# Kernel tuning notes

Hardware: AMD Instinct MI355X
Metric: run time of the kernel (lower is better)

## Reference

```python
import jax, jax.numpy as jnp
import numpy as np

B, L, D = 2, 4096, 1024
H, DK, DV = 4, 256, 256
CONV_K, FIR_S, FIR_L = 4, 3, 31
CHUNK = 32
EPS = 1e-5


def l2norm(x):
    return x * jax.lax.rsqrt(jnp.sum(x * x, -1, keepdims=True) + 1e-6)


def causal_dwconv(x, w):
    # x: [B, L, C], w: [C, K] depthwise causal FIR conv (left pad K-1)
    C, K = w.shape
    y = jax.lax.conv_general_dilated(
        jnp.swapaxes(x, 1, 2), w[:, None, :], (1,), [(K - 1, 0)],
        feature_group_count=C, dimension_numbers=('NCH', 'OIH', 'NCH'))
    return jnp.swapaxes(y, 1, 2)


def delta_rule_chunkwise(q, k, v, beta, chunk=CHUNK):
    # q,k: [b,h,L,dk], v: [b,h,L,dv], beta: [b,h,L]
    b, h, Lx, dk = q.shape
    dv = v.shape[-1]
    pad = (-Lx) % chunk
    if pad:
        q, k, v = (jnp.pad(t, ((0, 0), (0, 0), (0, pad), (0, 0))) for t in (q, k, v))
        beta = jnp.pad(beta, ((0, 0), (0, 0), (0, pad)))
    Lp = Lx + pad
    n = Lp // chunk
    q = l2norm(q)
    k = l2norm(k)
    v = v * beta[..., None]
    k_beta = k * beta[..., None]
    ch = lambda t: t.reshape(b, h, n, chunk, -1)
    qc, kc, vc, kbc = map(ch, (q, k, v, k_beta))
    # UT transform: T = (I + strictly_lower(k_beta @ k^T))^{-1}
    A = jnp.einsum('bhncd,bhned->bhnce', kbc, kc)
    eye = jnp.eye(chunk, dtype=q.dtype)
    T = jnp.linalg.inv(eye + jnp.tril(A, -1))  # same math as the sequential forward-substitution loop
    u = T @ vc      # [b,h,n,c,dv]
    w = T @ kbc     # [b,h,n,c,dk]
    tri = jnp.tril(jnp.ones((chunk, chunk), bool))  # causal incl. diagonal

    def body(S, inp):
        q_i, k_i, u_i, w_i = inp
        attn = jnp.where(tri, jnp.einsum('bhcd,bhed->bhce', q_i, k_i), 0.)
        u_i = u_i - w_i @ S
        o_i = q_i @ S + attn @ u_i
        S = S + jnp.einsum('bhcd,bhce->bhde', k_i, u_i)
        return S, o_i

    mv = lambda t: jnp.moveaxis(t, 2, 0)
    S0 = jnp.zeros((b, h, dk, dv), q.dtype)
    S, o = jax.lax.scan(body, S0, (mv(qc), mv(kc), mv(u), mv(w)))
    o = jnp.moveaxis(o, 0, 2).reshape(b, h, Lp, dv)[:, :, :Lx]
    return o, S


def setup_inputs() -> dict:
    key = jax.random.key(0)
    ks = jax.random.split(key, 16)
    s = 0.02
    fir_short = jnp.zeros((H, DV, FIR_S)).at[..., -1].set(1.0) + 1e-3 * jax.random.normal(ks[8], (H, DV, FIR_S))
    fir_long = jnp.zeros((H, DV, FIR_L)).at[..., -1].set(1.0) + 1e-3 * jax.random.normal(ks[9], (H, DV, FIR_L))
    bl = jnp.zeros((H, 3)).at[:, 0].set(2.0).reshape(-1)  # value_path_bias
    return dict(
        hidden_states=jax.random.normal(ks[0], (B, L, D), jnp.float32),
        Wq=s * jax.random.normal(ks[1], (D, H * DK)),
        Wk=s * jax.random.normal(ks[2], (D, H * DK)),
        Wv=s * jax.random.normal(ks[3], (D, H * DV)),
        conv_q=0.3 * jax.random.normal(ks[4], (H * DK, CONV_K)),
        conv_k=0.3 * jax.random.normal(ks[5], (H * DK, CONV_K)),
        conv_v=0.3 * jax.random.normal(ks[6], (H * DV, CONV_K)),
        Wb=s * jax.random.normal(ks[7], (D, H)),
        fir_short=fir_short,
        fir_long=fir_long,
        Wg=s * jax.random.normal(ks[10], (D, H)),
        bg=0.5 * jnp.ones((H,)),  # global_gate_bias
        Wl=s * jax.random.normal(ks[11], (D, H * 3)),
        bl=bl,
        log_temp=jnp.ones((H,)),  # log(e * temp_init) with temp_init=1
        rms_w=jnp.ones((DV,)),
        Wo=s * jax.random.normal(ks[12], (H * DV, D)),
    )


def reference(hidden_states, Wq, Wk, Wv, conv_q, conv_k, conv_v, Wb,
              fir_short, fir_long, Wg, bg, Wl, bl, log_temp, rms_w, Wo):
    x = hidden_states
    Bx, Lx, _ = x.shape
    # q/k/v projections + causal short conv + SiLU (qk_activation='silu')
    q = jax.nn.silu(causal_dwconv(x @ Wq, conv_q)).reshape(Bx, Lx, H, DK)
    k = jax.nn.silu(causal_dwconv(x @ Wk, conv_k)).reshape(Bx, Lx, H, DK)
    v = jax.nn.silu(causal_dwconv(x @ Wv, conv_v)).reshape(Bx, Lx, H, DV)
    beta = jax.nn.sigmoid(x @ Wb)  # [B,L,H]
    o_d, S = delta_rule_chunkwise(
        q.transpose(0, 2, 1, 3), k.transpose(0, 2, 1, 3),
        v.transpose(0, 2, 1, 3), beta.transpose(0, 2, 1))
    delta_out = o_d.transpose(0, 2, 1, 3)  # [B,L,H,DV]
    # local FIR paths on v (per-head depthwise causal FIR)
    vf = v.reshape(Bx, Lx, H * DV)
    local_short = causal_dwconv(vf, fir_short.reshape(H * DV, FIR_S)).reshape(Bx, Lx, H, DV)
    local_long = causal_dwconv(vf, fir_long.reshape(H * DV, FIR_L)).reshape(Bx, Lx, H, DV)
    # hierarchical two-stage gating with learnable per-head temperature
    w_global = jax.nn.sigmoid(x @ Wg + bg)  # [B,L,H]
    temp = jnp.exp(log_temp)                # [H]
    logits = (x @ Wl + bl).reshape(Bx, Lx, H, 3) / temp[:, None]
    p = jax.nn.softmax(logits, axis=-1)
    local_mix = p[..., 0:1] * v + p[..., 1:2] * local_short + p[..., 2:3] * local_long
    o = w_global[..., None] * delta_out + (1.0 - w_global)[..., None] * local_mix
    # per-head RMSNorm then output projection
    o = o * jax.lax.rsqrt(jnp.mean(o * o, -1, keepdims=True) + EPS) * rms_w
    return o.reshape(Bx, Lx, H * DV) @ Wo
```

## Files before the change

### kernel.cpp

```cpp
#include <hip/hip_runtime.h>
#include <hip/hip_bf16.h>
#include <math.h>

#define Bn 2
#define Ln 4096
#define Dn 1024
#define Hn 4
#define DKn 256
#define DVn 256
#define NCHn 128

typedef __attribute__((ext_vector_type(8))) short short8;
typedef __attribute__((ext_vector_type(4))) float f32x4;

__device__ __forceinline__ float sigmoidf_(float x) { return 1.f / (1.f + __expf(-x)); }

__device__ __forceinline__ unsigned short f2bf(float f) {
  union { float f; unsigned u; } v; v.f = f;
  unsigned r = v.u + 0x7FFFu + ((v.u >> 16) & 1u);
  return (unsigned short)(r >> 16);
}

__device__ __forceinline__ unsigned cvt_pk_bf16(float a, float b) {
  unsigned r;
  asm volatile("v_cvt_pk_bf16_f32 %0, %1, %2" : "=v"(r) : "v"(a), "v"(b));
  return r;
}

__device__ __forceinline__ short8 pack_i4(int4 o) {
  short8 r;
  __builtin_memcpy(&r, &o, 16);
  return r;
}

__device__ __forceinline__ void gl2lds16(const void* g, void* l) {
  __builtin_amdgcn_global_load_lds((const __attribute__((address_space(1))) unsigned int*)g,
                                   (__attribute__((address_space(3))) unsigned int*)l, 16, 0, 0);
}

__global__ __launch_bounds__(256) void wt_kernel(const float* __restrict__ W,
                                                 unsigned short* __restrict__ Wt,
                                                 int K, int N) {
  __shared__ float tile[32][33];
  const int bx = blockIdx.x * 32;
  const int by = blockIdx.y * 32;
  const int tx = threadIdx.x & 31, ty4 = (threadIdx.x >> 5) * 4;
#pragma unroll
  for (int r = 0; r < 4; ++r)
    tile[ty4 + r][tx] = W[(size_t)(by + ty4 + r) * N + bx + tx];
  __syncthreads();
#pragma unroll
  for (int r = 0; r < 4; ++r)
    Wt[(size_t)(bx + ty4 + r) * K + by + tx] = f2bf(tile[tx][ty4 + r]);
}

__global__ __launch_bounds__(256) void f2bf_kernel(const float* __restrict__ in,
                                                   unsigned short* __restrict__ out,
                                                   int n) {
  const int i4 = (blockIdx.x * 256 + threadIdx.x) * 4;
  if (i4 >= n) return;
  const float4 v = *(const float4*)&in[i4];
  ushort4 o;
  o.x = f2bf(v.x); o.y = f2bf(v.y); o.z = f2bf(v.z); o.w = f2bf(v.w);
  *(ushort4*)&out[i4] = o;
}

__global__ __launch_bounds__(256, 2) void gemm_bf16(const unsigned short* __restrict__ A,
                                                    const unsigned short* __restrict__ Bt,
                                                    float* __restrict__ C,
                                                    int M, int N, int K) {
  __shared__ __align__(16) unsigned short As[128 * 32];
  __shared__ __align__(16) unsigned short Bs[128 * 32];
  const int tid = threadIdx.x;
  const int wid = tid >> 6, lane = tid & 63;
  const int row0 = blockIdx.y * 128, col0 = blockIdx.x * 128;
  const int wr64 = (wid >> 1) * 64, wc64 = (wid & 1) * 64;
  const int fr = lane & 15, fg = lane >> 4;
  f32x4 acc[4][4];
#pragma unroll
  for (int i = 0; i < 4; ++i)
#pragma unroll
    for (int j = 0; j < 4; ++j) acc[i][j] = (f32x4){0.f, 0.f, 0.f, 0.f};
  for (int k0 = 0; k0 < K; k0 += 32) {
#pragma unroll
    for (int i = 0; i < 2; ++i) {
      const int off = wid * 2048 + i * 1024 + (lane << 4);
      const int r = off >> 6;
      const int kb = off & 63;
      gl2lds16((const char*)A + ((size_t)(row0 + r) * K + k0) * 2 + kb, (char*)As + off);
      gl2lds16((const char*)Bt + ((size_t)(col0 + r) * K + k0) * 2 + kb, (char*)Bs + off);
    }
    __syncthreads();
    short8 a[4], b[4];
#pragma unroll
    for (int mi = 0; mi < 4; ++mi)
      a[mi] = *(const short8*)&As[(wr64 + mi * 16 + fr) * 32 + fg * 8];
#pragma unroll
    for (int ni = 0; ni < 4; ++ni)
      b[ni] = *(const short8*)&Bs[(wc64 + ni * 16 + fr) * 32 + fg * 8];
#pragma unroll
    for (int mi = 0; mi < 4; ++mi)
#pragma unroll
      for (int ni = 0; ni < 4; ++ni)
        acc[mi][ni] = __builtin_amdgcn_mfma_f32_16x16x32_bf16(a[mi], b[ni], acc[mi][ni], 0, 0, 0);
    __syncthreads();
  }
#pragma unroll
  for (int mi = 0; mi < 4; ++mi) {
    const int orow = row0 + wr64 + mi * 16 + fg * 4;
#pragma unroll
    for (int ni = 0; ni < 4; ++ni) {
      const int ocol = col0 + wc64 + ni * 16 + fr;
#pragma unroll
      for (int r = 0; r < 4; ++r)
        C[(size_t)(orow + r) * N + ocol] = acc[mi][ni][r];
    }
  }
}

__global__ __launch_bounds__(256) void gates_kernel(
    const float* __restrict__ x, const float* __restrict__ Wb,
    const float* __restrict__ Wg, const float* __restrict__ bg,
    const float* __restrict__ Wl, const float* __restrict__ bl,
    const float* __restrict__ log_temp, float* __restrict__ beta,
    float* __restrict__ wgl, float* __restrict__ pmix) {
  const int wave = threadIdx.x >> 6, lane = threadIdx.x & 63;
  const int row = (blockIdx.x << 2) + wave;
  if (row >= Bn * Ln) return;
  const float* xr = x + (size_t)row * Dn;
  float acc[20];
#pragma unroll
  for (int c = 0; c < 20; ++c) acc[c] = 0.f;
#pragma unroll
  for (int i = 0; i < 4; ++i) {
    const float4 xv = *(const float4*)&xr[(lane << 2) + (i << 8)];
    const float xa[4] = {xv.x, xv.y, xv.z, xv.w};
#pragma unroll
    for (int j = 0; j < 4; ++j) {
      const int kk = (i << 8) + (lane << 2) + j;
      const float xx = xa[j];
#pragma unroll
      for (int h = 0; h < 4; ++h) acc[h] = fmaf(xx, Wb[kk * 4 + h], acc[h]);
#pragma unroll
      for (int h = 0; h < 4; ++h) acc[4 + h] = fmaf(xx, Wg[kk * 4 + h], acc[4 + h]);
#pragma unroll
      for (int c = 0; c < 12; ++c) acc[8 + c] = fmaf(xx, Wl[kk * 12 + c], acc[8 + c]);
    }
  }
#pragma unroll
  for (int c = 0; c < 20; ++c)
    for (int off = 32; off; off >>= 1) acc[c] += __shfl_down(acc[c], off);
  if (lane == 0) {
    const int b = row >> 12, l = row & (Ln - 1);
#pragma unroll
    for (int h = 0; h < 4; ++h)
      beta[((size_t)(b * Hn + h) << 12) + l] = sigmoidf_(acc[h]);
#pragma unroll
    for (int h = 0; h < 4; ++h) wgl[row * 4 + h] = sigmoidf_(acc[4 + h] + bg[h]);
#pragma unroll
    for (int h = 0; h < 4; ++h) {
      const float it = 1.f / __expf(log_temp[h]);
      const float l0 = (acc[8 + h * 3 + 0] + bl[h * 3 + 0]) * it;
      const float l1 = (acc[8 + h * 3 + 1] + bl[h * 3 + 1]) * it;
      const float l2 = (acc[8 + h * 3 + 2] + bl[h * 3 + 2]) * it;
      const float mx = fmaxf(l0, fmaxf(l1, l2));
      const float e0 = __expf(l0 - mx), e1 = __expf(l1 - mx), e2 = __expf(l2 - mx);
      const float is = 1.f / (e0 + e1 + e2);
      pmix[row * 12 + h * 3 + 0] = e0 * is;
      pmix[row * 12 + h * 3 + 1] = e1 * is;
      pmix[row * 12 + h * 3 + 2] = e2 * is;
    }
  }
}

template <int DO_L2>
__global__ __launch_bounds__(256) void conv_act_kernel(
    const float* __restrict__ raw, const float* __restrict__ cw,
    float* __restrict__ out, int coloff) {
  const int blk = blockIdx.x;
  const int b = blk >> 12, l = blk & (Ln - 1);
  const int t = threadIdx.x;
  float vals[4];
#pragma unroll
  for (int g = 0; g < 4; ++g) {
    const int c = (g << 8) + t;
    float a = 0.f;
#pragma unroll
    for (int j = 0; j < 4; ++j) {
      const int ls = l - 3 + j;
      if (ls >= 0)
        a = fmaf(cw[c * 4 + j], raw[(((size_t)b << 12) + ls) * 3072 + coloff + c], a);
    }
    vals[g] = a * sigmoidf_(a);
  }
  if (DO_L2) {
    __shared__ float red[4][4];
    float ss[4];
#pragma unroll
    for (int g = 0; g < 4; ++g) ss[g] = vals[g] * vals[g];
#pragma unroll
    for (int g = 0; g < 4; ++g)
      for (int off = 32; off; off >>= 1) ss[g] += __shfl_down(ss[g], off);
    const int wave = t >> 6, lane = t & 63;
    if (lane == 0) {
#pragma unroll
      for (int g = 0; g < 4; ++g) red[wave][g] = ss[g];
    }
    __syncthreads();
#pragma unroll
    for (int g = 0; g < 4; ++g) {
      const float s = red[0][g] + red[1][g] + red[2][g] + red[3][g];
      vals[g] *= rsqrtf(s + 1e-6f);
    }
  }
#pragma unroll
  for (int g = 0; g < 4; ++g)
    out[((((size_t)(b * Hn + g)) << 12) + l) * 256 + t] = vals[g];
}

__global__ __launch_bounds__(256, 2) void precomp_kernel(
    const float* __restrict__ q, const float* __restrict__ k,
    const float* __restrict__ v, const float* __restrict__ beta,
    unsigned short* __restrict__ wfrag, unsigned short* __restrict__ qfrag,
    unsigned short* __restrict__ ktfrag, unsigned short* __restrict__ afrag,
    float* __restrict__ u0frag) {
  const int blk = blockIdx.x;
  const int n = blk & 127, bh = blk >> 7;
  const size_t base = (((size_t)bh << 12) + (n << 5)) * 256;
  const size_t cid = (size_t)(bh * NCHn + n);
  __shared__ __align__(16) unsigned short ksb[32][264];
  __shared__ __align__(16) unsigned short qsb[32][264];
  __shared__ __align__(16) unsigned short vbb[32][264];
  __shared__ float Tm[32][33], Am[32][33], bet[32];
  __shared__ __align__(16) float attn_l[32][36];
  const int t = threadIdx.x;
  const int wid = t >> 6, lane = t & 63;
  const int fr = lane & 15, fg = lane >> 4;
  if (t < 32) bet[t] = beta[((size_t)bh << 12) + (n << 5) + t];
#pragma unroll
  for (int it = 0; it < 4; ++it) {
    const int idx = t + it * 256;
    const int r = idx >> 5, c8 = (idx & 31) << 3;
    const float bv = beta[((size_t)bh << 12) + (n << 5) + r];
    const float4 q0 = *(const float4*)&q[base + r * 256 + c8];
    const float4 q1 = *(const float4*)&q[base + r * 256 + c8 + 4];
    const float4 k0 = *(const float4*)&k[base + r * 256 + c8];
    const float4 k1 = *(const float4*)&k[base + r * 256 + c8 + 4];
    const float4 v0 = *(const float4*)&v[base + r * 256 + c8];
    const float4 v1 = *(const float4*)&v[base + r * 256 + c8 + 4];
    int4 oq, ok, ov;
    oq.x = cvt_pk_bf16(q0.x, q0.y); oq.y = cvt_pk_bf16(q0.z, q0.w);
    oq.z = cvt_pk_bf16(q1.x, q1.y); oq.w = cvt_pk_bf16(q1.z, q1.w);
    ok.x = cvt_pk_bf16(k0.x, k0.y); ok.y = cvt_pk_bf16(k0.z, k0.w);
    ok.z = cvt_pk_bf16(k1.x, k1.y); ok.w = cvt_pk_bf16(k1.z, k1.w);
    ov.x = cvt_pk_bf16(v0.x * bv, v0.y * bv); ov.y = cvt_pk_bf16(v0.z * bv, v0.w * bv);
    ov.z = cvt_pk_bf16(v1.x * bv, v1.y * bv); ov.w = cvt_pk_bf16(v1.z * bv, v1.w * bv);
    *(int4*)&qsb[r][c8] = oq;
    *(int4*)&ksb[r][c8] = ok;
    *(int4*)&vbb[r][c8] = ov;
  }
  __syncthreads();
  {
    const int ti = wid >> 1, tj = wid & 1;
    f32x4 G = (f32x4){0.f, 0.f, 0.f, 0.f};
    f32x4 At = (f32x4){0.f, 0.f, 0.f, 0.f};
#pragma unroll
    for (int kw = 0; kw < 8; ++kw) {
      const short8 krow = *(const short8*)&ksb[ti * 16 + fr][kw * 32 + fg * 8];
      const short8 kcol = *(const short8*)&ksb[tj * 16 + fr][kw * 32 + fg * 8];
      const short8 qrow = *(const short8*)&qsb[ti * 16 + fr][kw * 32 + fg * 8];
      G = __builtin_amdgcn_mfma_f32_16x16x32_bf16(krow, kcol, G, 0, 0, 0);
      At = __builtin_amdgcn_mfma_f32_16x16x32_bf16(qrow, kcol, At, 0, 0, 0);
    }
#pragma unroll
    for (int r_ = 0; r_ < 4; ++r_) {
      const int i = ti * 16 + fg * 4 + r_;
      const int j = tj * 16 + fr;
      Am[i][j] = bet[i] * G[r_];
      attn_l[i][j] = (j <= i) ? At[r_] : 0.f;
    }
  }
#pragma unroll
  for (int it = 0; it < 4; ++it) {
    const int u = it * 4 + wid;
    const int mi = u >> 3, kw = u & 7;
    *(int4*)&qfrag[cid * 8192 + u * 512 + lane * 8] =
        *(const int4*)&qsb[mi * 16 + fr][kw * 32 + fg * 8];
  }
#pragma unroll
  for (int it = 0; it < 4; ++it) {
    const int mi = it * 4 + wid;
    const int dk = mi * 16 + fr;
    unsigned short e[8];
#pragma unroll
    for (int j = 0; j < 8; ++j) e[j] = ksb[fg * 8 + j][dk];
    int4 o;
    o.x = e[0] | ((unsigned)e[1] << 16);
    o.y = e[2] | ((unsigned)e[3] << 16);
    o.z = e[4] | ((unsigned)e[5] << 16);
    o.w = e[6] | ((unsigned)e[7] << 16);
    *(int4*)&ktfrag[cid * 8192 + mi * 512 + lane * 8] = o;
  }
  __syncthreads();
  if (t >= 128) {
    const int mi = (t >> 6) - 2;
    const int c = mi * 16 + fr;
    const float4 a = *(const float4*)&attn_l[c][fg * 8];
    const float4 b2 = *(const float4*)&attn_l[c][fg * 8 + 4];
    int4 o;
    o.x = f2bf(a.x) | ((unsigned)f2bf(a.y) << 16);
    o.y = f2bf(a.z) | ((unsigned)f2bf(a.w) << 16);
    o.z = f2bf(b2.x) | ((unsigned)f2bf(b2.y) << 16);
    o.w = f2bf(b2.z) | ((unsigned)f2bf(b2.w) << 16);
    *(int4*)&afrag[cid * 1024 + mi * 512 + lane * 8] = o;
  }
  if (t < 32) {
    float Tcol[32];
    Tcol[0] = (t == 0) ? 1.f : 0.f;
#pragma unroll
    for (int i = 1; i < 32; ++i) {
      float s0 = 0.f, s1 = 0.f;
      int m = 0;
#pragma unroll
      for (; m + 2 <= i; m += 2) {
        s0 = fmaf(Am[i][m], Tcol[m], s0);
        s1 = fmaf(Am[i][m + 1], Tcol[m + 1], s1);
      }
      if (m < i) s0 = fmaf(Am[i][m], Tcol[m], s0);
      Tcol[i] = ((i == t) ? 1.f : 0.f) - s0 - s1;
    }
#pragma unroll
    for (int i = 0; i < 32; ++i) Tm[i][t] = Tcol[i];
  }
  __syncthreads();
  {
    float betr[8];
#pragma unroll
    for (int j = 0; j < 8; ++j) betr[j] = bet[fg * 8 + j];
    short8 Tf[2], Tbf[2];
#pragma unroll
    for (int mi = 0; mi < 2; ++mi) {
      float tv[8];
#pragma unroll
      for (int j = 0; j < 8; ++j) tv[j] = Tm[mi * 16 + fr][fg * 8 + j];
      int4 p, pb;
      p.x = cvt_pk_bf16(tv[0], tv[1]); p.y = cvt_pk_bf16(tv[2], tv[3]);
      p.z = cvt_pk_bf16(tv[4], tv[5]); p.w = cvt_pk_bf16(tv[6], tv[7]);
      pb.x = cvt_pk_bf16(tv[0] * betr[0], tv[1] * betr[1]);
      pb.y = cvt_pk_bf16(tv[2] * betr[2], tv[3] * betr[3]);
      pb.z = cvt_pk_bf16(tv[4] * betr[4], tv[5] * betr[5]);
      pb.w = cvt_pk_bf16(tv[6] * betr[6], tv[7] * betr[7]);
      Tf[mi] = pack_i4(p);
      Tbf[mi] = pack_i4(pb);
    }
    const f32x4 zero = (f32x4){0.f, 0.f, 0.f, 0.f};
#pragma unroll
    for (int tt = 0; tt < 4; ++tt) {
      const int tjc = wid * 4 + tt;
      unsigned short ev[8], ek[8];
#pragma unroll
      for (int j = 0; j < 8; ++j) {
        ev[j] = vbb[fg * 8 + j][tjc * 16 + fr];
        ek[j] = ksb[fg * 8 + j][tjc * 16 + fr];
      }
      int4 pv, pk;
      pv.x = ev[0] | ((unsigned)ev[1] << 16); pv.y = ev[2] | ((unsigned)ev[3] << 16);
      pv.z = ev[4] | ((unsigned)ev[5] << 16); pv.w = ev[6] | ((unsigned)ev[7] << 16);
      pk.x = ek[0] | ((unsigned)ek[1] << 16); pk.y = ek[2] | ((unsigned)ek[3] << 16);
      pk.z = ek[4] | ((unsigned)ek[5] << 16); pk.w = ek[6] | ((unsigned)ek[7] << 16);
      const short8 vbf = pack_i4(pv);
      const short8 kbf = pack_i4(pk);
#pragma unroll
      for (int mi = 0; mi < 2; ++mi) {
        const f32x4 U = __builtin_amdgcn_mfma_f32_16x16x32_bf16(Tf[mi], vbf, zero, 0, 0, 0);
        *(f32x4*)&u0frag[cid * 8192 + (tjc * 2 + mi) * 256 + lane * 4] = U;
        const f32x4 W = __builtin_amdgcn_mfma_f32_16x16x32_bf16(Tbf[mi], kbf, zero, 0, 0, 0);
#pragma unroll
        for (int r_ = 0; r_ < 4; ++r_)
          qsb[mi * 16 + fg * 4 + r_][tjc * 16 + fr] = f2bf(W[r_]);
      }
    }
  }
  __syncthreads();
#pragma unroll
  for (int it = 0; it < 4; ++it) {
    const int u = it * 4 + wid;
    const int mi = u >> 3, kw = u & 7;
    *(int4*)&wfrag[cid * 8192 + u * 512 + lane * 8] =
        *(const int4*)&qsb[mi * 16 + fr][kw * 32 + fg * 8];
  }
}

__global__ __launch_bounds__(128, 1) void scan_mfma(
    const unsigned short* __restrict__ wfrag, const unsigned short* __restrict__ qfrag,
    const unsigned short* __restrict__ ktfrag, const unsigned short* __restrict__ afrag,
    const float* __restrict__ u0frag, float* __restrict__ dout) {
  const int bh = blockIdx.x & 7;
  const int dvs = blockIdx.x >> 3;
  const int tid = threadIdx.x;
  const int w = tid >> 6;
  const int lane = tid & 63;
  const int fr = lane & 15, fg = lane >> 4;
  const int swz = (fr & 7) << 4;
  __shared__ __align__(16) unsigned short St[2][2048];
  __shared__ __align__(16) unsigned short ut2[2][512];
  __shared__ __align__(16) float pux[2][2][2][256];
  __shared__ __align__(16) float pox[2][2][2][256];
  f32x4 S[8];
#pragma unroll
  for (int i = 0; i < 8; ++i) S[i] = (f32x4){0.f, 0.f, 0.f, 0.f};

  const unsigned short* wbase = wfrag + (size_t)(bh * NCHn) * 8192;
  const unsigned short* qbase = qfrag + (size_t)(bh * NCHn) * 8192;
  const unsigned short* kbase = ktfrag + (size_t)(bh * NCHn) * 8192;
  const unsigned short* abase = afrag + (size_t)(bh * NCHn) * 1024;
  const float* ubase = u0frag + (size_t)(bh * NCHn) * 8192 + dvs * 512;

  short8 wr[8], qr[8], ktr[8];
  short8 ar[2] = {};
  f32x4 u0r[2];
#pragma unroll
  for (int u8 = 0; u8 < 8; ++u8) {
    const int mi = u8 >> 2, kwp = u8 & 3;
    const int u = mi * 8 + 4 * w + kwp;
    wr[u8] = *(const short8*)&wbase[u * 512 + lane * 8];
    qr[u8] = *(const short8*)&qbase[u * 512 + lane * 8];
    ktr[u8] = *(const short8*)&kbase[(8 * w + u8) * 512 + lane * 8];
  }
#pragma unroll
  for (int u = 0; u < 2; ++u) u0r[u] = *(const f32x4*)&ubase[u * 256 + lane * 4];
  if (w == 0) {
#pragma unroll
    for (int u = 0; u < 2; ++u) ar[u] = *(const short8*)&abase[u * 512 + lane * 8];
  }

  for (int n = 0; n < NCHn; ++n) {
    const int np = (n + 1 < NCHn) ? (n + 1) : n;
    const int buf = n & 1;
#pragma unroll
    for (int mi = 0; mi < 8; ++mi) {
      const unsigned w0 = cvt_pk_bf16(S[mi][0], S[mi][1]);
      const unsigned w1 = cvt_pk_bf16(S[mi][2], S[mi][3]);
      const int a = (fr * 256 + mi * 32 + fg * 8) ^ swz;
      *(uint2*)((char*)&St[w][0] + a) = make_uint2(w0, w1);
    }
    short8 sb[4];
#pragma unroll
    for (int kwp = 0; kwp < 4; ++kwp) {
      const int a = (fr * 256 + kwp * 64 + fg * 16) ^ swz;
      sb[kwp] = *(const short8*)((const char*)&St[w][0] + a);
    }
    f32x4 up[2], oq[2];
    up[0] = up[1] = (f32x4){0.f, 0.f, 0.f, 0.f};
    oq[0] = oq[1] = (f32x4){0.f, 0.f, 0.f, 0.f};
#pragma unroll
    for (int kwp = 0; kwp < 4; ++kwp) {
#pragma unroll
      for (int mi = 0; mi < 2; ++mi) {
        up[mi] = __builtin_amdgcn_mfma_f32_16x16x32_bf16(wr[mi * 4 + kwp], sb[kwp], up[mi], 0, 0, 0);
        oq[mi] = __builtin_amdgcn_mfma_f32_16x16x32_bf16(qr[mi * 4 + kwp], sb[kwp], oq[mi], 0, 0, 0);
      }
    }
    {
      const unsigned short* wp = wbase + (size_t)np * 8192;
      const unsigned short* qp = qbase + (size_t)np * 8192;
#pragma unroll
      for (int u8 = 0; u8 < 8; ++u8) {
        const int mi = u8 >> 2, kwp = u8 & 3;
        const int u = mi * 8 + 4 * w + kwp;
        wr[u8] = *(const short8*)&wp[u * 512 + lane * 8];
        qr[u8] = *(const short8*)&qp[u * 512 + lane * 8];
      }
    }
#pragma unroll
    for (int mi = 0; mi < 2; ++mi) {
      *(f32x4*)&pux[w][buf][mi][lane * 4] = up[mi];
      *(f32x4*)&pox[w][buf][mi][lane * 4] = oq[mi];
    }
    asm volatile("s_waitcnt lgkmcnt(0)" ::: "memory");
    __builtin_amdgcn_s_barrier();
    __builtin_amdgcn_sched_barrier(0);
    f32x4 o_f[2];
#pragma unroll
    for (int mi = 0; mi < 2; ++mi) {
      const f32x4 puo = *(const f32x4*)&pux[w ^ 1][buf][mi][lane * 4];
      const f32x4 uu = u0r[mi] - up[mi] - puo;
      const unsigned a0 = cvt_pk_bf16(uu[0], uu[1]);
      const unsigned a1 = cvt_pk_bf16(uu[2], uu[3]);
      const int ad = (fr * 64 + mi * 32 + fg * 8) ^ swz;
      *(uint2*)((char*)&ut2[w][0] + ad) = make_uint2(a0, a1);
      o_f[mi] = oq[mi] + *(const f32x4*)&pox[w ^ 1][buf][mi][lane * 4];
    }
    asm volatile("s_waitcnt lgkmcnt(0)" ::: "memory");
    __builtin_amdgcn_sched_barrier(0);
    const short8 ub = *(const short8*)((const char*)&ut2[w][0] + ((fr * 64 + fg * 16) ^ swz));
    if (w == 0) {
#pragma unroll
      for (int mi = 0; mi < 2; ++mi)
        o_f[mi] = __builtin_amdgcn_mfma_f32_16x16x32_bf16(ar[mi], ub, o_f[mi], 0, 0, 0);
      const unsigned short* ap = abase + (size_t)np * 1024;
#pragma unroll
      for (int u = 0; u < 2; ++u) ar[u] = *(const short8*)&ap[u * 512 + lane * 8];
      const size_t cb = ((size_t)((bh << 12) + (n << 5))) * 256;
#pragma unroll
      for (int mi = 0; mi < 2; ++mi)
#pragma unroll
        for (int r = 0; r < 4; ++r)
          dout[cb + (size_t)(mi * 16 + fg * 4 + r) * 256 + dvs * 16 + fr] = o_f[mi][r];
    }
    {
      const float* up_ = ubase + (size_t)np * 8192;
#pragma unroll
      for (int u = 0; u < 2; ++u) u0r[u] = *(const f32x4*)&up_[u * 256 + lane * 4];
    }
#pragma unroll
    for (int mi = 0; mi < 8; ++mi)
      S[mi] = __builtin_amdgcn_mfma_f32_16x16x32_bf16(ktr[mi], ub, S[mi], 0, 0, 0);
    {
      const unsigned short* kp = kbase + (size_t)np * 8192;
#pragma unroll
      for (int u8 = 0; u8 < 8; ++u8)
        ktr[u8] = *(const short8*)&kp[(8 * w + u8) * 512 + lane * 8];
    }
  }
}

#define MIX_LT 16
__global__ __launch_bounds__(256) void mix_kernel(
    const float* __restrict__ v, const float* __restrict__ delta,
    const float* __restrict__ wgl, const float* __restrict__ pmix,
    const float* __restrict__ firs, const float* __restrict__ firl,
    const float* __restrict__ rms_w, unsigned short* __restrict__ out) {
  const int wgid = ((int)blockIdx.x & 7) * 256 + ((int)blockIdx.x >> 3);
  const int b = wgid >> 10;
  const int h = (wgid >> 8) & 3;
  const int lt = wgid & 255;
  const int l0 = lt * MIX_LT;
  const int t = threadIdx.x;
  const int wv = t >> 6, lane = t & 63;
  const float* vcol = v + ((((size_t)(b * Hn + h)) << 12)) * 256 + t;
  const float* dcol = delta + ((((size_t)(b * Hn + h)) << 12)) * 256 + t;
  float fw[31], fs3[3];
#pragma unroll
  for (int j = 0; j < 31; ++j) fw[j] = firl[((h << 8) + t) * 31 + j];
#pragma unroll
  for (int j = 0; j < 3; ++j) fs3[j] = firs[((h << 8) + t) * 3 + j];
  const float rw = rms_w[t];
  float vbuf[46];
#pragma unroll
  for (int j = 0; j < 30; ++j) {
    const int ls = l0 - 30 + j;
    vbuf[j] = (ls >= 0) ? vcol[(size_t)ls * 256] : 0.f;
  }
#pragma unroll
  for (int i = 0; i < MIX_LT; ++i) vbuf[30 + i] = vcol[(size_t)(l0 + i) * 256];
  __shared__ float wred[MIX_LT * 4];
  float o[MIX_LT];
#pragma unroll
  for (int i = 0; i < MIX_LT; ++i) {
    const int l = l0 + i;
    const float vnew = vbuf[30 + i];
    float lo = fw[30] * vnew;
#pragma unroll
    for (int j = 0; j < 30; ++j) lo = fmaf(fw[j], vbuf[i + j], lo);
    float sh = fs3[2] * vnew;
    sh = fmaf(fs3[1], vbuf[i + 29], sh);
    sh = fmaf(fs3[0], vbuf[i + 28], sh);
    const int row = (b << 12) + l;
    const float p0 = pmix[row * 12 + h * 3 + 0];
    const float p1 = pmix[row * 12 + h * 3 + 1];
    const float p2 = pmix[row * 12 + h * 3 + 2];
    const float wg = wgl[row * 4 + h];
    const float mixv = p0 * vnew + p1 * sh + p2 * lo;
    const float oo = wg * dcol[(size_t)l * 256] + (1.f - wg) * mixv;
    o[i] = oo;
    float ss = oo * oo;
#pragma unroll
    for (int m = 1; m < 64; m <<= 1) ss += __shfl_xor(ss, m);
    if (lane == 0) wred[i * 4 + wv] = ss;
  }
  __syncthreads();
#pragma unroll
  for (int i = 0; i < MIX_LT; ++i) {
    const float sum = wred[i * 4] + wred[i * 4 + 1] + wred[i * 4 + 2] + wred[i * 4 + 3];
    const float sc = rsqrtf(sum * (1.f / 256.f) + 1e-5f);
    const int l = l0 + i;
    out[(size_t)((b << 12) + l) * 1024 + (h << 8) + t] = f2bf(o[i] * sc * rw);
  }
}

extern "C" void kernel_launch(void* const* d_in, const int* in_sizes, int n_in,
                              void* d_out, int out_size, void* d_ws, size_t ws_size,
                              hipStream_t stream) {
  const float* x = (const float*)d_in[0];
  const float* Wq = (const float*)d_in[1];
  const float* Wk = (const float*)d_in[2];
  const float* Wv = (const float*)d_in[3];
  const float* cq = (const float*)d_in[4];
  const float* ck = (const float*)d_in[5];
  const float* cv = (const float*)d_in[6];
  const float* Wb = (const float*)d_in[7];
  const float* firs = (const float*)d_in[8];
  const float* firl = (const float*)d_in[9];
  const float* Wg = (const float*)d_in[10];
  const float* bg = (const float*)d_in[11];
  const float* Wl = (const float*)d_in[12];
  const float* bl = (const float*)d_in[13];
  const float* ltemp = (const float*)d_in[14];
  const float* rmsw = (const float*)d_in[15];
  const float* Wo = (const float*)d_in[16];

  float* ws = (float*)d_ws;
  const size_t NE = (size_t)Bn * Ln * 1024;
  float* qkvraw = ws;
  float* kraw = ws + NE;
  float* vraw = ws + 2 * NE;
  float* qn = ws + 3 * NE;
  float* kn = ws + 4 * NE;
  float* vn = ws + 5 * NE;
  float* beta = ws + 6 * NE;
  float* wgl = beta + (size_t)Bn * Hn * Ln;
  float* pmix = wgl + (size_t)Bn * Ln * Hn;
  float* attn_unused = pmix + (size_t)Bn * Ln * Hn * 3;
  unsigned short* Wot = (unsigned short*)(attn_unused + (size_t)Bn * Hn * NCHn * 1024);
  unsigned short* xb = (unsigned short*)qn;
  unsigned short* Wqt = (unsigned short*)(qn + 4194304);
  unsigned short* Wkt = Wqt + 1048576;
  unsigned short* Wvt = Wkt + 1048576;
  unsigned short* normed_bf = (unsigned short*)kn;
  unsigned short* wfrag = (unsigned short*)qkvraw;
  unsigned short* qfrag = wfrag + 8388608;
  unsigned short* ktfrag = (unsigned short*)kraw;
  unsigned short* afrag = ktfrag + 8388608;
  float* u0frag = qn;
  float* dbuf = vraw;

  const dim3 wtg(32, 32);
  wt_kernel<<<wtg, 256, 0, stream>>>(Wq, Wqt, 1024, 1024);
  wt_kernel<<<wtg, 256, 0, stream>>>(Wk, Wkt, 1024, 1024);
  wt_kernel<<<wtg, 256, 0, stream>>>(Wv, Wvt, 1024, 1024);
  wt_kernel<<<wtg, 256, 0, stream>>>(Wo, Wot, 1024, 1024);
  f2bf_kernel<<<(int)(NE / 1024), 256, 0, stream>>>(x, xb, (int)NE);

  gemm_bf16<<<dim3(24, 64), 256, 0, stream>>>(xb, Wqt, qkvraw, Bn * Ln, 3072, 1024);
  gates_kernel<<<Bn * Ln / 4, 256, 0, stream>>>(x, Wb, Wg, bg, Wl, bl, ltemp,
                                                beta, wgl, pmix);
  conv_act_kernel<1><<<Bn * Ln, 256, 0, stream>>>(qkvraw, cq, qn, 0);
  conv_act_kernel<1><<<Bn * Ln, 256, 0, stream>>>(qkvraw, ck, kn, 1024);
  conv_act_kernel<0><<<Bn * Ln, 256, 0, stream>>>(qkvraw, cv, vn, 2048);
  precomp_kernel<<<Bn * Hn * NCHn, 256, 0, stream>>>(qn, kn, vn, beta, wfrag,
                                                     qfrag, ktfrag, afrag, u0frag);
  scan_mfma<<<128, 128, 0, stream>>>(wfrag, qfrag, ktfrag, afrag, u0frag, dbuf);
  mix_kernel<<<Bn * Hn * (Ln / MIX_LT), 256, 0, stream>>>(
      vn, dbuf, wgl, pmix, firs, firl, rmsw, normed_bf);
  gemm_bf16<<<dim3(8, 64), 256, 0, stream>>>(normed_bf, Wot, (float*)d_out,
                                             Bn * Ln, 1024, 1024);
}
```

Before: 458.4 us.

## Store intermediates in bf16 and fuse weight transposes and x conversion

Stores the QKV projection output, the conv-activated q/k/v, and the delta-rule output as bf16 instead of fp32, roughly halving intermediate memory traffic across the conv, precompute, scan and mix kernels. The four weight-transpose launches are merged into one 3D-grid kernel, and the x-to-bf16 conversion is folded into the gates kernel, removing a standalone pass. The workspace layout is reorganised to match. This adds bf16 rounding before the conv/SiLU/L2 norm and before the mix, which could reduce accuracy.

Result: faster. 444.6 us (-3.0%).

```diff
diff --git a/kernel.cpp b/kernel.cpp
--- a/kernel.cpp
+++ b/kernel.cpp
@@ -21,6 +21,11 @@
   return (unsigned short)(r >> 16);
 }
 
+__device__ __forceinline__ float bf2f(unsigned short u) {
+  union { unsigned u; float f; } v; v.u = ((unsigned)u) << 16;
+  return v.f;
+}
+
 __device__ __forceinline__ unsigned cvt_pk_bf16(float a, float b) {
   unsigned r;
   asm volatile("v_cvt_pk_bf16_f32 %0, %1, %2" : "=v"(r) : "v"(a), "v"(b));
@@ -38,36 +43,32 @@
                                    (__attribute__((address_space(3))) unsigned int*)l, 16, 0, 0);
 }
 
-__global__ __launch_bounds__(256) void wt_kernel(const float* __restrict__ W,
-                                                 unsigned short* __restrict__ Wt,
-                                                 int K, int N) {
+__global__ __launch_bounds__(256) void wt_all_kernel(
+    const float* __restrict__ W0, const float* __restrict__ W1,
+    const float* __restrict__ W2, const float* __restrict__ W3,
+    unsigned short* __restrict__ T0, unsigned short* __restrict__ T1,
+    unsigned short* __restrict__ T2, unsigned short* __restrict__ T3) {
+  const float* W = (blockIdx.z == 0) ? W0 : (blockIdx.z == 1) ? W1
+                   : (blockIdx.z == 2) ? W2 : W3;
+  unsigned short* Wt = (blockIdx.z == 0) ? T0 : (blockIdx.z == 1) ? T1
+                       : (blockIdx.z == 2) ? T2 : T3;
   __shared__ float tile[32][33];
   const int bx = blockIdx.x * 32;
   const int by = blockIdx.y * 32;
   const int tx = threadIdx.x & 31, ty4 = (threadIdx.x >> 5) * 4;
 #pragma unroll
   for (int r = 0; r < 4; ++r)
-    tile[ty4 + r][tx] = W[(size_t)(by + ty4 + r) * N + bx + tx];
+    tile[ty4 + r][tx] = W[(size_t)(by + ty4 + r) * 1024 + bx + tx];
   __syncthreads();
 #pragma unroll
   for (int r = 0; r < 4; ++r)
-    Wt[(size_t)(bx + ty4 + r) * K + by + tx] = f2bf(tile[tx][ty4 + r]);
-}
-
-__global__ __launch_bounds__(256) void f2bf_kernel(const float* __restrict__ in,
-                                                   unsigned short* __restrict__ out,
-                                                   int n) {
-  const int i4 = (blockIdx.x * 256 + threadIdx.x) * 4;
-  if (i4 >= n) return;
-  const float4 v = *(const float4*)&in[i4];
-  ushort4 o;
-  o.x = f2bf(v.x); o.y = f2bf(v.y); o.z = f2bf(v.z); o.w = f2bf(v.w);
-  *(ushort4*)&out[i4] = o;
-}
-
+    Wt[(size_t)(bx + ty4 + r) * 1024 + by + tx] = f2bf(tile[tx][ty4 + r]);
+}
+
+template <int OBF>
 __global__ __launch_bounds__(256, 2) void gemm_bf16(const unsigned short* __restrict__ A,
                                                     const unsigned short* __restrict__ Bt,
-                                                    float* __restrict__ C,
+                                                    void* __restrict__ Cv,
                                                     int M, int N, int K) {
   __shared__ __align__(16) unsigned short As[128 * 32];
   __shared__ __align__(16) unsigned short Bs[128 * 32];
@@ -111,9 +112,17 @@
 #pragma unroll
     for (int ni = 0; ni < 4; ++ni) {
       const int ocol = col0 + wc64 + ni * 16 + fr;
-#pragma unroll
-      for (int r = 0; r < 4; ++r)
-        C[(size_t)(orow + r) * N + ocol] = acc[mi][ni][r];
+      if (OBF) {
+        unsigned short* C = (unsigned short*)Cv;
+#pragma unroll
+        for (int r = 0; r < 4; ++r)
+          C[(size_t)(orow + r) * N + ocol] = f2bf(acc[mi][ni][r]);
+      } else {
+        float* C = (float*)Cv;
+#pragma unroll
+        for (int r = 0; r < 4; ++r)
+          C[(size_t)(orow + r) * N + ocol] = acc[mi][ni][r];
+      }
     }
   }
 }
@@ -123,7 +132,8 @@
     const float* __restrict__ Wg, const float* __restrict__ bg,
     const float* __restrict__ Wl, const float* __restrict__ bl,
     const float* __restrict__ log_temp, float* __restrict__ beta,
-    float* __restrict__ wgl, float* __restrict__ pmix) {
+    float* __restrict__ wgl, float* __restrict__ pmix,
+    unsigned short* __restrict__ xb) {
   const int wave = threadIdx.x >> 6, lane = threadIdx.x & 63;
   const int row = (blockIdx.x << 2) + wave;
   if (row >= Bn * Ln) return;
@@ -134,6 +144,9 @@
 #pragma unroll
   for (int i = 0; i < 4; ++i) {
     const float4 xv = *(const float4*)&xr[(lane << 2) + (i << 8)];
+    ushort4 ob;
+    ob.x = f2bf(xv.x); ob.y = f2bf(xv.y); ob.z = f2bf(xv.z); ob.w = f2bf(xv.w);
+    *(ushort4*)&xb[(size_t)row * Dn + (i << 8) + (lane << 2)] = ob;
     const float xa[4] = {xv.x, xv.y, xv.z, xv.w};
 #pragma unroll
     for (int j = 0; j < 4; ++j) {
@@ -175,8 +188,8 @@
 
 template <int DO_L2>
 __global__ __launch_bounds__(256) void conv_act_kernel(
-    const float* __restrict__ raw, const float* __restrict__ cw,
-    float* __restrict__ out, int coloff) {
+    const unsigned short* __restrict__ raw, const float* __restrict__ cw,
+    unsigned short* __restrict__ out, int coloff) {
   const int blk = blockIdx.x;
   const int b = blk >> 12, l = blk & (Ln - 1);
   const int t = threadIdx.x;
@@ -189,7 +202,7 @@
     for (int j = 0; j < 4; ++j) {
       const int ls = l - 3 + j;
       if (ls >= 0)
-        a = fmaf(cw[c * 4 + j], raw[(((size_t)b << 12) + ls) * 3072 + coloff + c], a);
+        a = fmaf(cw[c * 4 + j], bf2f(raw[(((size_t)b << 12) + ls) * 3072 + coloff + c]), a);
     }
     vals[g] = a * sigmoidf_(a);
   }
@@ -215,12 +228,12 @@
   }
 #pragma unroll
   for (int g = 0; g < 4; ++g)
-    out[((((size_t)(b * Hn + g)) << 12) + l) * 256 + t] = vals[g];
+    out[((((size_t)(b * Hn + g)) << 12) + l) * 256 + t] = f2bf(vals[g]);
 }
 
 __global__ __launch_bounds__(256, 2) void precomp_kernel(
-    const float* __restrict__ q, const float* __restrict__ k,
-    const float* __restrict__ v, const float* __restrict__ beta,
+    const unsigned short* __restrict__ q, const unsigned short* __restrict__ k,
+    const unsigned short* __restrict__ v, const float* __restrict__ beta,
     unsigned short* __restrict__ wfrag, unsigned short* __restrict__ qfrag,
     unsigned short* __restrict__ ktfrag, unsigned short* __restrict__ afrag,
     float* __restrict__ u0frag) {
@@ -242,21 +255,19 @@
     const int idx = t + it * 256;
     const int r = idx >> 5, c8 = (idx & 31) << 3;
     const float bv = beta[((size_t)bh << 12) + (n << 5) + r];
-    const float4 q0 = *(const float4*)&q[base + r * 256 + c8];
-    const float4 q1 = *(const float4*)&q[base + r * 256 + c8 + 4];
-    const float4 k0 = *(const float4*)&k[base + r * 256 + c8];
-    const float4 k1 = *(const float4*)&k[base + r * 256 + c8 + 4];
-    const float4 v0 = *(const float4*)&v[base + r * 256 + c8];
-    const float4 v1 = *(const float4*)&v[base + r * 256 + c8 + 4];
-    int4 oq, ok, ov;
-    oq.x = cvt_pk_bf16(q0.x, q0.y); oq.y = cvt_pk_bf16(q0.z, q0.w);
-    oq.z = cvt_pk_bf16(q1.x, q1.y); oq.w = cvt_pk_bf16(q1.z, q1.w);
-    ok.x = cvt_pk_bf16(k0.x, k0.y); ok.y = cvt_pk_bf16(k0.z, k0.w);
-    ok.z = cvt_pk_bf16(k1.x, k1.y); ok.w = cvt_pk_bf16(k1.z, k1.w);
-    ov.x = cvt_pk_bf16(v0.x * bv, v0.y * bv); ov.y = cvt_pk_bf16(v0.z * bv, v0.w * bv);
-    ov.z = cvt_pk_bf16(v1.x * bv, v1.y * bv); ov.w = cvt_pk_bf16(v1.z * bv, v1.w * bv);
-    *(int4*)&qsb[r][c8] = oq;
-    *(int4*)&ksb[r][c8] = ok;
+    *(int4*)&qsb[r][c8] = *(const int4*)&q[base + r * 256 + c8];
+    *(int4*)&ksb[r][c8] = *(const int4*)&k[base + r * 256 + c8];
+    const int4 vv = *(const int4*)&v[base + r * 256 + c8];
+    const unsigned vu[4] = {(unsigned)vv.x, (unsigned)vv.y, (unsigned)vv.z, (unsigned)vv.w};
+    int4 ov;
+    ov.x = cvt_pk_bf16(bf2f((unsigned short)(vu[0] & 0xffff)) * bv,
+                       bf2f((unsigned short)(vu[0] >> 16)) * bv);
+    ov.y = cvt_pk_bf16(bf2f((unsigned short)(vu[1] & 0xffff)) * bv,
+                       bf2f((unsigned short)(vu[1] >> 16)) * bv);
+    ov.z = cvt_pk_bf16(bf2f((unsigned short)(vu[2] & 0xffff)) * bv,
+                       bf2f((unsigned short)(vu[2] >> 16)) * bv);
+    ov.w = cvt_pk_bf16(bf2f((unsigned short)(vu[3] & 0xffff)) * bv,
+                       bf2f((unsigned short)(vu[3] >> 16)) * bv);
     *(int4*)&vbb[r][c8] = ov;
   }
   __syncthreads();
@@ -394,7 +405,7 @@
 __global__ __launch_bounds__(128, 1) void scan_mfma(
     const unsigned short* __restrict__ wfrag, const unsigned short* __restrict__ qfrag,
     const unsigned short* __restrict__ ktfrag, const unsigned short* __restrict__ afrag,
-    const float* __restrict__ u0frag, float* __restrict__ dout) {
+    const float* __restrict__ u0frag, unsigned short* __restrict__ dout) {
   const int bh = blockIdx.x & 7;
   const int dvs = blockIdx.x >> 3;
   const int tid = threadIdx.x;
@@ -506,7 +517,7 @@
       for (int mi = 0; mi < 2; ++mi)
 #pragma unroll
         for (int r = 0; r < 4; ++r)
-          dout[cb + (size_t)(mi * 16 + fg * 4 + r) * 256 + dvs * 16 + fr] = o_f[mi][r];
+          dout[cb + (size_t)(mi * 16 + fg * 4 + r) * 256 + dvs * 16 + fr] = f2bf(o_f[mi][r]);
     }
     {
       const float* up_ = ubase + (size_t)np * 8192;
@@ -527,7 +538,7 @@
 
 #define MIX_LT 16
 __global__ __launch_bounds__(256) void mix_kernel(
-    const float* __restrict__ v, const float* __restrict__ delta,
+    const unsigned short* __restrict__ v, const unsigned short* __restrict__ delta,
     const float* __restrict__ wgl, const float* __restrict__ pmix,
     const float* __restrict__ firs, const float* __restrict__ firl,
     const float* __restrict__ rms_w, unsigned short* __restrict__ out) {
@@ -538,8 +549,8 @@
   const int l0 = lt * MIX_LT;
   const int t = threadIdx.x;
   const int wv = t >> 6, lane = t & 63;
-  const float* vcol = v + ((((size_t)(b * Hn + h)) << 12)) * 256 + t;
-  const float* dcol = delta + ((((size_t)(b * Hn + h)) << 12)) * 256 + t;
+  const unsigned short* vcol = v + ((((size_t)(b * Hn + h)) << 12)) * 256 + t;
+  const unsigned short* dcol = delta + ((((size_t)(b * Hn + h)) << 12)) * 256 + t;
   float fw[31], fs3[3];
 #pragma unroll
   for (int j = 0; j < 31; ++j) fw[j] = firl[((h << 8) + t) * 31 + j];
@@ -550,10 +561,10 @@
 #pragma unroll
   for (int j = 0; j < 30; ++j) {
     const int ls = l0 - 30 + j;
-    vbuf[j] = (ls >= 0) ? vcol[(size_t)ls * 256] : 0.f;
-  }
-#pragma unroll
-  for (int i = 0; i < MIX_LT; ++i) vbuf[30 + i] = vcol[(size_t)(l0 + i) * 256];
+    vbuf[j] = (ls >= 0) ? bf2f(vcol[(size_t)ls * 256]) : 0.f;
+  }
+#pragma unroll
+  for (int i = 0; i < MIX_LT; ++i) vbuf[30 + i] = bf2f(vcol[(size_t)(l0 + i) * 256]);
   __shared__ float wred[MIX_LT * 4];
   float o[MIX_LT];
 #pragma unroll
@@ -572,7 +583,7 @@
     const float p2 = pmix[row * 12 + h * 3 + 2];
     const float wg = wgl[row * 4 + h];
     const float mixv = p0 * vnew + p1 * sh + p2 * lo;
-    const float oo = wg * dcol[(size_t)l * 256] + (1.f - wg) * mixv;
+    const float oo = wg * bf2f(dcol[(size_t)l * 256]) + (1.f - wg) * mixv;
     o[i] = oo;
     float ss = oo * oo;
 #pragma unroll
@@ -612,47 +623,40 @@
 
   float* ws = (float*)d_ws;
   const size_t NE = (size_t)Bn * Ln * 1024;
-  float* qkvraw = ws;
-  float* kraw = ws + NE;
-  float* vraw = ws + 2 * NE;
-  float* qn = ws + 3 * NE;
-  float* kn = ws + 4 * NE;
-  float* vn = ws + 5 * NE;
+  unsigned short* qkvbf = (unsigned short*)ws;
+  unsigned short* wfrag = (unsigned short*)ws;
+  unsigned short* qfrag = wfrag + 8388608;
+  unsigned short* ktfrag = (unsigned short*)(ws + NE);
+  unsigned short* afrag = ktfrag + 8388608;
+  float* u0frag = ws + 2 * NE;
+  unsigned short* xb = (unsigned short*)(ws + 3 * NE);
+  unsigned short* normed_bf = xb;
+  unsigned short* Wqt = xb + NE;
+  unsigned short* Wkt = Wqt + 1048576;
+  unsigned short* Wvt = Wkt + 1048576;
+  unsigned short* qn_bf = (unsigned short*)(ws + 4 * NE);
+  unsigned short* kn_bf = qn_bf + NE;
+  unsigned short* vn_bf = (unsigned short*)(ws + 5 * NE);
+  unsigned short* dout_bf = vn_bf + NE;
   float* beta = ws + 6 * NE;
   float* wgl = beta + (size_t)Bn * Hn * Ln;
   float* pmix = wgl + (size_t)Bn * Ln * Hn;
-  float* attn_unused = pmix + (size_t)Bn * Ln * Hn * 3;
-  unsigned short* Wot = (unsigned short*)(attn_unused + (size_t)Bn * Hn * NCHn * 1024);
-  unsigned short* xb = (unsigned short*)qn;
-  unsigned short* Wqt = (unsigned short*)(qn + 4194304);
-  unsigned short* Wkt = Wqt + 1048576;
-  unsigned short* Wvt = Wkt + 1048576;
-  unsigned short* normed_bf = (unsigned short*)kn;
-  unsigned short* wfrag = (unsigned short*)qkvraw;
-  unsigned short* qfrag = wfrag + 8388608;
-  unsigned short* ktfrag = (unsigned short*)kraw;
-  unsigned short* afrag = ktfrag + 8388608;
-  float* u0frag = qn;
-  float* dbuf = vraw;
-
-  const dim3 wtg(32, 32);
-  wt_kernel<<<wtg, 256, 0, stream>>>(Wq, Wqt, 1024, 1024);
-  wt_kernel<<<wtg, 256, 0, stream>>>(Wk, Wkt, 1024, 1024);
-  wt_kernel<<<wtg, 256, 0, stream>>>(Wv, Wvt, 1024, 1024);
-  wt_kernel<<<wtg, 256, 0, stream>>>(Wo, Wot, 1024, 1024);
-  f2bf_kernel<<<(int)(NE / 1024), 256, 0, stream>>>(x, xb, (int)NE);
-
-  gemm_bf16<<<dim3(24, 64), 256, 0, stream>>>(xb, Wqt, qkvraw, Bn * Ln, 3072, 1024);
+  unsigned short* Wot = (unsigned short*)(pmix + (size_t)Bn * Ln * Hn * 3);
+
+  wt_all_kernel<<<dim3(32, 32, 4), 256, 0, stream>>>(Wq, Wk, Wv, Wo,
+                                                     Wqt, Wkt, Wvt, Wot);
   gates_kernel<<<Bn * Ln / 4, 256, 0, stream>>>(x, Wb, Wg, bg, Wl, bl, ltemp,
-                                                beta, wgl, pmix);
-  conv_act_kernel<1><<<Bn * Ln, 256, 0, stream>>>(qkvraw, cq, qn, 0);
-  conv_act_kernel<1><<<Bn * Ln, 256, 0, stream>>>(qkvraw, ck, kn, 1024);
-  conv_act_kernel<0><<<Bn * Ln, 256, 0, stream>>>(qkvraw, cv, vn, 2048);
-  precomp_kernel<<<Bn * Hn * NCHn, 256, 0, stream>>>(qn, kn, vn, beta, wfrag,
-                                                     qfrag, ktfrag, afrag, u0frag);
-  scan_mfma<<<128, 128, 0, stream>>>(wfrag, qfrag, ktfrag, afrag, u0frag, dbuf);
+                                                beta, wgl, pmix, xb);
+  gemm_bf16<1><<<dim3(24, 64), 256, 0, stream>>>(xb, Wqt, qkvbf, Bn * Ln, 3072, 1024);
+  conv_act_kernel<1><<<Bn * Ln, 256, 0, stream>>>(qkvbf, cq, qn_bf, 0);
+  conv_act_kernel<1><<<Bn * Ln, 256, 0, stream>>>(qkvbf, ck, kn_bf, 1024);
+  conv_act_kernel<0><<<Bn * Ln, 256, 0, stream>>>(qkvbf, cv, vn_bf, 2048);
+  precomp_kernel<<<Bn * Hn * NCHn, 256, 0, stream>>>(qn_bf, kn_bf, vn_bf, beta,
+                                                     wfrag, qfrag, ktfrag, afrag,
+                                                     u0frag);
+  scan_mfma<<<128, 128, 0, stream>>>(wfrag, qfrag, ktfrag, afrag, u0frag, dout_bf);
   mix_kernel<<<Bn * Hn * (Ln / MIX_LT), 256, 0, stream>>>(
-      vn, dbuf, wgl, pmix, firs, firl, rmsw, normed_bf);
-  gemm_bf16<<<dim3(8, 64), 256, 0, stream>>>(normed_bf, Wot, (float*)d_out,
-                                             Bn * Ln, 1024, 1024);
-}
+      vn_bf, dout_bf, wgl, pmix, firs, firl, rmsw, normed_bf);
+  gemm_bf16<0><<<dim3(8, 64), 256, 0, stream>>>(normed_bf, Wot, (float*)d_out,
+                                                Bn * Ln, 1024, 1024);
+}
```
